# Kernel tuning notes

Measured on AMD Instinct MI355X. Metric: run time of the kernel, lower is better.

## Reference

```python
import jax, jax.numpy as jnp
import numpy as np

DEPTH = 8            # 2**DEPTH - 1 = 255 internal nodes, 2**DEPTH = 256 leaves
BATCH = 2048
NUM_CLASSES = 200
EPS = 1e-07


def setup_inputs() -> dict:
    key = jax.random.key(0)
    k_sim, k_leaf = jax.random.split(key)
    # similarities[i] is the LOG prob of routing right at internal node i
    # (heap order: children of i are 2i+1, 2i+2). Log-probs are <= 0.
    sims = -(jax.random.uniform(k_sim, (2 ** DEPTH - 1, BATCH), dtype=jnp.float32) * 3.0 + 0.01)
    leaf_logits = jax.random.normal(k_leaf, (2 ** DEPTH, NUM_CLASSES), dtype=jnp.float32)
    return {"similarities": sims, "leaf_logits": leaf_logits}


def reference(similarities, leaf_logits):
    B = similarities.shape[1]
    C = leaf_logits.shape[1]
    log2 = jnp.asarray(np.log(2.0), dtype=similarities.dtype)
    # Leaf log-distributions, broadcast over batch: [n_leaves, B, C]
    dists = jnp.broadcast_to(jax.nn.log_softmax(leaf_logits, axis=-1)[:, None, :],
                             (leaf_logits.shape[0], B, C))
    # Bottom-up over tree levels (fixed small loop over DEPTH levels).
    for level in reversed(range(DEPTH)):
        n = 2 ** level
        p_right = similarities[n - 1: 2 * n - 1][:, :, None]   # [n, B, 1]
        a = jnp.abs(p_right) + EPS
        # numerically-stable log(1 - exp(-a)), split at log(2) as in the source
        p_left = jnp.where(a < log2,
                           jnp.log(-jnp.expm1(-a)),
                           jnp.log1p(-jnp.exp(-a)))
        # children of level-l node j are the consecutive pair (2j, 2j+1) in level l+1
        dists = jnp.logaddexp(p_left + dists[0::2], p_right + dists[1::2])  # [n, B, C]
    return dists[0]  # root pred_logits: [B, C]
```

## Files before the change

kernel.cpp:

```cpp
#include <hip/hip_runtime.h>

#define DEPTH 8
#define NINT 255
#define NLEAF 256
#define BATCH 2048
#define NCLS 200
#define EPS 1e-7f
#define TB 8
#define LPAD 264
#define NTILE 13

typedef float f32x4 __attribute__((ext_vector_type(4)));
typedef __bf16 bf16x8 __attribute__((ext_vector_type(8)));

static __device__ __forceinline__ unsigned short f2bf(float f) {
    unsigned int u = __builtin_bit_cast(unsigned int, f);
    return (unsigned short)((u + 0x8000u) >> 16);
}

__global__ __launch_bounds__(256) void tree_fused(
    const float* __restrict__ sims, const float* __restrict__ logits,
    float* __restrict__ out) {
    __shared__ unsigned short Et[(NTILE * 16) * LPAD];
    __shared__ unsigned short Wt[16 * LPAD];
    __shared__ float pr_s[NINT * TB];
    __shared__ float pl_s[NINT * TB];
    __shared__ float invZ[NLEAF];

    const int tid = threadIdx.x;
    const int b0 = blockIdx.x * TB;

    float prv[8];
#pragma unroll
    for (int p = 0; p < 8; ++p) {
        const int idx = tid + 256 * p;
        if (idx < NINT * TB)
            prv[p] = sims[(idx >> 3) * BATCH + b0 + (idx & 7)];
    }

    {
        unsigned int* wz = (unsigned int*)(Wt + 8 * LPAD);
        unsigned int* ez = (unsigned int*)(Et + 200 * LPAD);
        for (int i = tid; i < (8 * LPAD) / 2; i += 256) { wz[i] = 0u; ez[i] = 0u; }
    }

    {
        const float4* lr = (const float4*)(logits + tid * NCLS);
        float Z = 0.f;
        for (int j = 0; j < NCLS / 4; ++j) {
            const float4 v = lr[j];
            const float e0 = __expf(v.x), e1 = __expf(v.y),
                        e2 = __expf(v.z), e3 = __expf(v.w);
            Z += (e0 + e1) + (e2 + e3);
            const int c = 4 * j;
            Et[(c + 0) * LPAD + tid] = f2bf(e0);
            Et[(c + 1) * LPAD + tid] = f2bf(e1);
            Et[(c + 2) * LPAD + tid] = f2bf(e2);
            Et[(c + 3) * LPAD + tid] = f2bf(e3);
        }
        invZ[tid] = __builtin_amdgcn_rcpf(Z);
    }

#pragma unroll
    for (int p = 0; p < 8; ++p) {
        const int idx = tid + 256 * p;
        if (idx < NINT * TB) {
            const float pr = prv[p];
            const float pl = __logf(1.0f - __expf(pr - EPS));
            pr_s[idx] = pr;
            pl_s[idx] = pl;
        }
    }
    __syncthreads();

#pragma unroll
    for (int p = 0; p < 8; ++p) {
        const int idx = tid + 256 * p;
        const int l = idx >> 3;
        const int b = idx & 7;
        float w = 0.f;
        int n = NINT + l;
#pragma unroll
        for (int d = 0; d < DEPTH; ++d) {
            const int par = (n - 1) >> 1;
            w += ((n & 1) == 0) ? pr_s[par * TB + b] : pl_s[par * TB + b];
            n = par;
        }
        Wt[b * LPAD + l] = f2bf(__expf(w) * invZ[l]);
    }
    __syncthreads();

    const int lane = tid & 63;
    const int wave = tid >> 6;
    const int mn = lane & 15;
    const int quad = lane >> 4;

    f32x4 acc0 = {0.f, 0.f, 0.f, 0.f};
    f32x4 acc1 = {0.f, 0.f, 0.f, 0.f};
    f32x4 acc2 = {0.f, 0.f, 0.f, 0.f};
    f32x4 acc3 = {0.f, 0.f, 0.f, 0.f};
    const int t0 = wave, t1 = wave + 4, t2 = wave + 8, t3 = wave + 12;

#pragma unroll
    for (int s = 0; s < 8; ++s) {
        const int ko = s * 32 + quad * 8;
        const bf16x8 a = *(const bf16x8*)(Wt + mn * LPAD + ko);
        const bf16x8 bv0 = *(const bf16x8*)(Et + (t0 * 16 + mn) * LPAD + ko);
        acc0 = __builtin_amdgcn_mfma_f32_16x16x32_bf16(a, bv0, acc0, 0, 0, 0);
        const bf16x8 bv1 = *(const bf16x8*)(Et + (t1 * 16 + mn) * LPAD + ko);
        acc1 = __builtin_amdgcn_mfma_f32_16x16x32_bf16(a, bv1, acc1, 0, 0, 0);
        const bf16x8 bv2 = *(const bf16x8*)(Et + (t2 * 16 + mn) * LPAD + ko);
        acc2 = __builtin_amdgcn_mfma_f32_16x16x32_bf16(a, bv2, acc2, 0, 0, 0);
        if (wave == 0) {
            const bf16x8 bv3 = *(const bf16x8*)(Et + (t3 * 16 + mn) * LPAD + ko);
            acc3 = __builtin_amdgcn_mfma_f32_16x16x32_bf16(a, bv3, acc3, 0, 0, 0);
        }
    }

    if (quad < 2) {
        const int rbase = b0 + quad * 4;
#pragma unroll
        for (int i = 0; i < 4; ++i) {
            const int t = (i == 0) ? t0 : (i == 1) ? t1 : (i == 2) ? t2 : t3;
            if (t >= NTILE) continue;
            const f32x4 acc = (i == 0) ? acc0 : (i == 1) ? acc1
                            : (i == 2) ? acc2 : acc3;
            const int c = t * 16 + mn;
            if (c < NCLS) {
#pragma unroll
                for (int r = 0; r < 4; ++r)
                    out[(size_t)(rbase + r) * NCLS + c] = __logf(acc[r]);
            }
        }
    }
}

extern "C" void kernel_launch(void* const* d_in, const int* in_sizes, int n_in,
                              void* d_out, int out_size, void* d_ws, size_t ws_size,
                              hipStream_t stream) {
    const float* sims = (const float*)d_in[0];
    const float* logits = (const float*)d_in[1];
    float* out = (float*)d_out;
    tree_fused<<<BATCH / TB, 256, 0, stream>>>(sims, logits, out);
}
```

Measured before the change: 70.78 us.

## Split leaf softmax into a separate kernel and read bf16 leaf table from global

The leaf softmax, which every one of the 256 blocks previously recomputed into shared memory, now runs once in a small pre-kernel. That kernel writes a normalized bf16 transposed table to the workspace. The GEMM kernel then streams its B operand straight from global memory (L2-resident) and prefetches the first k-slice before the tree-weight computation. This removes redundant exp work and a large LDS footprint, which may raise occupancy. The cost is a second launch and global loads inside the MFMA loop.

```diff
diff --git a/kernel.cpp b/kernel.cpp
--- a/kernel.cpp
+++ b/kernel.cpp
@@ -18,14 +18,39 @@
     return (unsigned short)((u + 0x8000u) >> 16);
 }
 
-__global__ __launch_bounds__(256) void tree_fused(
-    const float* __restrict__ sims, const float* __restrict__ logits,
+__global__ __launch_bounds__(64) void leaf_softmax(
+    const float* __restrict__ logits, unsigned short* __restrict__ Et) {
+    const int l = blockIdx.x;
+    const int lane = threadIdx.x;
+    const float* row = logits + l * NCLS;
+
+    float e[4];
+    float Z = 0.f;
+#pragma unroll
+    for (int j = 0; j < 4; ++j) {
+        const int c = lane + 64 * j;
+        e[j] = (c < NCLS) ? __expf(row[c]) : 0.f;
+        Z += e[j];
+    }
+#pragma unroll
+    for (int off = 32; off >= 1; off >>= 1)
+        Z += __shfl_xor(Z, off);
+    const float invZ = __builtin_amdgcn_rcpf(Z);
+
+#pragma unroll
+    for (int j = 0; j < 4; ++j) {
+        const int c = lane + 64 * j;
+        if (c < NCLS) Et[c * NLEAF + l] = f2bf(e[j] * invZ);
+    }
+    if (lane < 8) Et[(NCLS + lane) * NLEAF + l] = 0;
+}
+
+__global__ __launch_bounds__(256) void tree_gemm(
+    const float* __restrict__ sims, const unsigned short* __restrict__ Et,
     float* __restrict__ out) {
-    __shared__ unsigned short Et[(NTILE * 16) * LPAD];
     __shared__ unsigned short Wt[16 * LPAD];
     __shared__ float pr_s[NINT * TB];
     __shared__ float pl_s[NINT * TB];
-    __shared__ float invZ[NLEAF];
 
     const int tid = threadIdx.x;
     const int b0 = blockIdx.x * TB;
@@ -38,27 +63,20 @@
             prv[p] = sims[(idx >> 3) * BATCH + b0 + (idx & 7)];
     }
 
+    const int lane = tid & 63;
+    const int wave = tid >> 6;
+    const int mn = lane & 15;
+    const int quad = lane >> 4;
+    const int t0 = wave, t1 = wave + 4, t2 = wave + 8, t3 = wave + 12;
+
+    const bf16x8 pb0 = *(const bf16x8*)(Et + (t0 * 16 + mn) * NLEAF + quad * 8);
+    const bf16x8 pb1 = *(const bf16x8*)(Et + (t1 * 16 + mn) * NLEAF + quad * 8);
+    const bf16x8 pb2 = *(const bf16x8*)(Et + (t2 * 16 + mn) * NLEAF + quad * 8);
+    const bf16x8 pb3 = *(const bf16x8*)(Et + (t3 * 16 + mn) * NLEAF * (t3 < NTILE) + quad * 8);
+
     {
         unsigned int* wz = (unsigned int*)(Wt + 8 * LPAD);
-        unsigned int* ez = (unsigned int*)(Et + 200 * LPAD);
-        for (int i = tid; i < (8 * LPAD) / 2; i += 256) { wz[i] = 0u; ez[i] = 0u; }
-    }
-
-    {
-        const float4* lr = (const float4*)(logits + tid * NCLS);
-        float Z = 0.f;
-        for (int j = 0; j < NCLS / 4; ++j) {
-            const float4 v = lr[j];
-            const float e0 = __expf(v.x), e1 = __expf(v.y),
-                        e2 = __expf(v.z), e3 = __expf(v.w);
-            Z += (e0 + e1) + (e2 + e3);
-            const int c = 4 * j;
-            Et[(c + 0) * LPAD + tid] = f2bf(e0);
-            Et[(c + 1) * LPAD + tid] = f2bf(e1);
-            Et[(c + 2) * LPAD + tid] = f2bf(e2);
-            Et[(c + 3) * LPAD + tid] = f2bf(e3);
-        }
-        invZ[tid] = __builtin_amdgcn_rcpf(Z);
+        for (int i = tid; i < (8 * LPAD) / 2; i += 256) wz[i] = 0u;
     }
 
 #pragma unroll
@@ -86,33 +104,31 @@
             w += ((n & 1) == 0) ? pr_s[par * TB + b] : pl_s[par * TB + b];
             n = par;
         }
-        Wt[b * LPAD + l] = f2bf(__expf(w) * invZ[l]);
+        Wt[b * LPAD + l] = f2bf(__expf(w));
     }
     __syncthreads();
-
-    const int lane = tid & 63;
-    const int wave = tid >> 6;
-    const int mn = lane & 15;
-    const int quad = lane >> 4;
 
     f32x4 acc0 = {0.f, 0.f, 0.f, 0.f};
     f32x4 acc1 = {0.f, 0.f, 0.f, 0.f};
     f32x4 acc2 = {0.f, 0.f, 0.f, 0.f};
     f32x4 acc3 = {0.f, 0.f, 0.f, 0.f};
-    const int t0 = wave, t1 = wave + 4, t2 = wave + 8, t3 = wave + 12;
 
 #pragma unroll
     for (int s = 0; s < 8; ++s) {
         const int ko = s * 32 + quad * 8;
         const bf16x8 a = *(const bf16x8*)(Wt + mn * LPAD + ko);
-        const bf16x8 bv0 = *(const bf16x8*)(Et + (t0 * 16 + mn) * LPAD + ko);
+        const bf16x8 bv0 = (s == 0) ? pb0
+                         : *(const bf16x8*)(Et + (t0 * 16 + mn) * NLEAF + ko);
         acc0 = __builtin_amdgcn_mfma_f32_16x16x32_bf16(a, bv0, acc0, 0, 0, 0);
-        const bf16x8 bv1 = *(const bf16x8*)(Et + (t1 * 16 + mn) * LPAD + ko);
+        const bf16x8 bv1 = (s == 0) ? pb1
+                         : *(const bf16x8*)(Et + (t1 * 16 + mn) * NLEAF + ko);
         acc1 = __builtin_amdgcn_mfma_f32_16x16x32_bf16(a, bv1, acc1, 0, 0, 0);
-        const bf16x8 bv2 = *(const bf16x8*)(Et + (t2 * 16 + mn) * LPAD + ko);
+        const bf16x8 bv2 = (s == 0) ? pb2
+                         : *(const bf16x8*)(Et + (t2 * 16 + mn) * NLEAF + ko);
         acc2 = __builtin_amdgcn_mfma_f32_16x16x32_bf16(a, bv2, acc2, 0, 0, 0);
         if (wave == 0) {
-            const bf16x8 bv3 = *(const bf16x8*)(Et + (t3 * 16 + mn) * LPAD + ko);
+            const bf16x8 bv3 = (s == 0) ? pb3
+                             : *(const bf16x8*)(Et + (t3 * 16 + mn) * NLEAF + ko);
             acc3 = __builtin_amdgcn_mfma_f32_16x16x32_bf16(a, bv3, acc3, 0, 0, 0);
         }
     }
@@ -141,5 +157,8 @@
     const float* sims = (const float*)d_in[0];
     const float* logits = (const float*)d_in[1];
     float* out = (float*)d_out;
-    tree_fused<<<BATCH / TB, 256, 0, stream>>>(sims, logits, out);
+    unsigned short* Et = (unsigned short*)d_ws;
+
+    leaf_softmax<<<NLEAF, 64, 0, stream>>>(logits, Et);
+    tree_gemm<<<BATCH / TB, 256, 0, stream>>>(sims, Et, out);
 }
```

After: 66.82 us. 5.6% less time.
